# Kernel optimization log

Hardware: AMD Instinct MI355X
Metric: run time of the kernel (lower is better)

Reference implementation:

```python
import jax, jax.numpy as jnp
import numpy as np

B, S, HID = 4, 2048, 2048
H, KV, D = 16, 4, 128
G = H // KV  # kv groups
EPS = 1e-6
SCALE = D ** -0.5


def setup_inputs() -> dict:
    key = jax.random.key(0)
    ks = jax.random.split(key, 8)
    hidden_states = jax.random.normal(ks[0], (B, S, HID), jnp.float32)
    # real RoPE tables (rotate-half convention: freqs duplicated across halves)
    inv_freq = 1.0 / (10000.0 ** (np.arange(0, D, 2, dtype=np.float32) / D))
    t = np.arange(S, dtype=np.float32)
    freqs = np.outer(t, inv_freq)                      # [S, D/2]
    emb = np.concatenate([freqs, freqs], axis=-1)      # [S, D]
    cos = jnp.asarray(np.cos(emb), jnp.float32)
    sin = jnp.asarray(np.sin(emb), jnp.float32)
    std = HID ** -0.5
    Wq = jax.random.normal(ks[1], (HID, H * D), jnp.float32) * std
    Wk = jax.random.normal(ks[2], (HID, KV * D), jnp.float32) * std
    Wv = jax.random.normal(ks[3], (HID, KV * D), jnp.float32) * std
    Wo = jax.random.normal(ks[4], (H * D, HID), jnp.float32) * std
    q_norm_w = jnp.ones((D,), jnp.float32)
    k_norm_w = jnp.ones((D,), jnp.float32)
    return {"hidden_states": hidden_states, "cos": cos, "sin": sin,
            "Wq": Wq, "Wk": Wk, "Wv": Wv, "Wo": Wo,
            "q_norm_w": q_norm_w, "k_norm_w": k_norm_w}


def _rms_norm(x, w):
    xf = x.astype(jnp.float32)
    var = jnp.mean(xf * xf, axis=-1, keepdims=True)
    return w * (xf * jax.lax.rsqrt(var + EPS)).astype(x.dtype)


def _rotate_half(x):
    x1, x2 = x[..., : D // 2], x[..., D // 2:]
    return jnp.concatenate([-x2, x1], axis=-1)


def reference(hidden_states, cos, sin, Wq, Wk, Wv, Wo, q_norm_w, k_norm_w):
    x = hidden_states  # [B, S, HID]
    # projections + per-head RMSNorm
    q = _rms_norm((x @ Wq).reshape(B, S, H, D), q_norm_w).transpose(0, 2, 1, 3)   # [B,H,S,D]
    k = _rms_norm((x @ Wk).reshape(B, S, KV, D), k_norm_w).transpose(0, 2, 1, 3)  # [B,KV,S,D]
    v = (x @ Wv).reshape(B, S, KV, D).transpose(0, 2, 1, 3)                        # [B,KV,S,D]
    # RoPE (cos/sin broadcast [S,D] -> [B,heads,S,D])
    q = q * cos + _rotate_half(q) * sin
    k = k * cos + _rotate_half(k) * sin
    # GQA attention without materializing expanded K/V: group q heads per kv head
    qg = q.reshape(B, KV, G, S, D)
    scores = jnp.einsum('bkgsd,bktd->bkgst', qg, k) * SCALE       # [B,KV,G,S,S]
    probs = jax.nn.softmax(scores, axis=-1)
    out = jnp.einsum('bkgst,bktd->bkgsd', probs, v)               # [B,KV,G,S,D]
    out = out.reshape(B, H, S, D).transpose(0, 2, 1, 3).reshape(B, S, H * D)
    return out @ Wo
```

## Files before the change

kernel.cpp:

```cpp
#include <hip/hip_runtime.h>

#define DEVI __device__ __forceinline__

#define B_    4
#define S_    2048
#define HID_  2048
#define H_    16
#define KV_   4
#define D_    128
#define NQKV_ 3072
#define SCALE_ 0.08838834764831845f
#define L2E_   1.44269504088896340736f

typedef __bf16 bf16x8 __attribute__((ext_vector_type(8)));
typedef float  f32x4  __attribute__((ext_vector_type(4)));
typedef unsigned short ushort_t;

DEVI unsigned short f2bu(float f) {
  unsigned u = __float_as_uint(f);
  u += 0x7fffu + ((u >> 16) & 1u);
  return (unsigned short)(u >> 16);
}
DEVI float bu2f(unsigned short s) { return __uint_as_float(((unsigned)s) << 16); }
DEVI unsigned pk2(float a, float b) {
  return (unsigned)f2bu(a) | ((unsigned)f2bu(b) << 16);
}

DEVI void storev(ushort_t* p, float v) { *p = f2bu(v); }
DEVI void storev(float* p, float v)    { *p = v; }

DEVI void gl_lds16(const void* gptr, void* ldsptr) {
  __builtin_amdgcn_global_load_lds(
      (const __attribute__((address_space(1))) void*)gptr,
      (__attribute__((address_space(3))) void*)ldsptr, 16, 0, 0);
}

__global__ void k_cvt(const float* __restrict__ in, ushort_t* __restrict__ out, int n8) {
  int i = blockIdx.x * blockDim.x + threadIdx.x;
  if (i >= n8) return;
  const float4* p = (const float4*)in + (size_t)i * 2;
  float4 a = p[0], b = p[1];
  uint4 o;
  o.x = pk2(a.x, a.y);
  o.y = pk2(a.z, a.w);
  o.z = pk2(b.x, b.y);
  o.w = pk2(b.z, b.w);
  ((uint4*)out)[i] = o;
}

__global__ void k_transw(const float* __restrict__ in, ushort_t* __restrict__ out,
                         int K, int N) {
  __shared__ float tile[64][65];
  int k0 = blockIdx.x * 64, n0 = blockIdx.y * 64;
  int c = threadIdx.x & 63, r0 = threadIdx.x >> 6;
  #pragma unroll
  for (int i = 0; i < 16; ++i) {
    int r = r0 * 16 + i;
    tile[r][c] = in[(size_t)(k0 + r) * N + n0 + c];
  }
  __syncthreads();
  #pragma unroll
  for (int i = 0; i < 16; ++i) {
    int r = r0 * 16 + i;
    out[(size_t)(n0 + r) * K + k0 + c] = f2bu(tile[c][r]);
  }
}

__global__ void k_vtrans(const ushort_t* __restrict__ qkv, ushort_t* __restrict__ Vt) {
  __shared__ ushort_t tile[64][65];
  int s0 = blockIdx.x * 64, d0 = blockIdx.y * 64;
  int bkv = blockIdx.z, b = bkv >> 2, vh = bkv & 3;
  int c = threadIdx.x & 63, r0 = (threadIdx.x >> 6) * 16;
  const ushort_t* src = qkv + (size_t)(b * S_ + s0) * NQKV_ + 2560 + vh * 128 + d0;
  #pragma unroll
  for (int i = 0; i < 16; ++i) {
    int r = r0 + i;
    tile[r][c] = src[(size_t)r * NQKV_ + c];
  }
  __syncthreads();
  ushort_t* dst = Vt + ((size_t)(b * KV_ + vh) * D_ + d0) * S_ + s0;
  #pragma unroll
  for (int i = 0; i < 16; ++i) {
    int r = r0 + i;
    dst[(size_t)r * S_ + c] = tile[c][r];
  }
}

template <typename OutT>
__global__ __launch_bounds__(256)
void k_gemm(const ushort_t* __restrict__ A, const ushort_t* __restrict__ Bt,
            OutT* __restrict__ C, int M, int N, int K) {
  __shared__ __align__(16) ushort_t As[128 * 64];
  __shared__ __align__(16) ushort_t Bs[128 * 64];
  const int tid = threadIdx.x;
  const int wave = tid >> 6, lane = tid & 63;
  const int wr = wave >> 1, wc = wave & 1;
  const int h4 = lane >> 4, c16 = lane & 15;
  const int m0 = blockIdx.x * 128, n0 = blockIdx.y * 128;

  const int srow  = wave * 8 + (lane >> 3);
  const int scolb = (lane & 7) * 16;

  const ushort_t* Ap = A  + (size_t)m0 * K;
  const ushort_t* Bp = Bt + (size_t)n0 * K;

  f32x4 acc[4][4] = {};

  for (int kt = 0; kt < K; kt += 64) {
    __syncthreads();
    #pragma unroll
    for (int p = 0; p < 4; ++p) {
      int row = p * 32 + srow;
      gl_lds16((const char*)(Ap + (size_t)row * K + kt) + scolb,
               (char*)As + p * 4096 + wave * 1024);
      gl_lds16((const char*)(Bp + (size_t)row * K + kt) + scolb,
               (char*)Bs + p * 4096 + wave * 1024);
    }
    __syncthreads();
    #pragma unroll
    for (int kc = 0; kc < 2; ++kc) {
      bf16x8 af[4], bfr[4];
      #pragma unroll
      for (int m = 0; m < 4; ++m)
        af[m] = *(const bf16x8*)((const char*)As + (wr * 64 + m * 16 + c16) * 128 + kc * 64 + h4 * 16);
      #pragma unroll
      for (int n = 0; n < 4; ++n)
        bfr[n] = *(const bf16x8*)((const char*)Bs + (wc * 64 + n * 16 + c16) * 128 + kc * 64 + h4 * 16);
      #pragma unroll
      for (int m = 0; m < 4; ++m)
        #pragma unroll
        for (int n = 0; n < 4; ++n)
          acc[m][n] = __builtin_amdgcn_mfma_f32_16x16x32_bf16(af[m], bfr[n], acc[m][n], 0, 0, 0);
    }
  }
  #pragma unroll
  for (int m = 0; m < 4; ++m)
    #pragma unroll
    for (int n = 0; n < 4; ++n)
      #pragma unroll
      for (int r = 0; r < 4; ++r) {
        int grow = m0 + wr * 64 + m * 16 + h4 * 4 + r;
        int gcol = n0 + wc * 64 + n * 16 + c16;
        storev(&C[(size_t)grow * N + gcol], acc[m][n][r]);
      }
}

__global__ void k_normrope(const ushort_t* __restrict__ qkv,
                           const float* __restrict__ cosT, const float* __restrict__ sinT,
                           const float* __restrict__ qw, const float* __restrict__ kw,
                           ushort_t* __restrict__ Qr,
                           ushort_t* __restrict__ Kr) {
  int wid = blockIdx.x * 4 + (threadIdx.x >> 6);
  int lane = threadIdx.x & 63;
  int sub = wid % 20;
  int bs = wid / 20;
  int b = bs >> 11, s = bs & 2047;
  bool isQ = sub < 16;
  int head = isQ ? sub : sub - 16;
  const ushort_t* rp = qkv + (size_t)bs * NQKV_ + (isQ ? head * 128 : 2048 + head * 128);
  float e0 = bu2f(rp[lane]);
  float e1 = bu2f(rp[lane + 64]);
  float ss2 = e0 * e0 + e1 * e1;
  #pragma unroll
  for (int off = 32; off; off >>= 1) ss2 += __shfl_xor(ss2, off);
  float rinv = rsqrtf(ss2 * (1.0f / 128.0f) + 1e-6f);
  const float* w = isQ ? qw : kw;
  float y0 = e0 * rinv * w[lane];
  float y1 = e1 * rinv * w[lane + 64];
  float c0 = cosT[s * 128 + lane],      sn0 = sinT[s * 128 + lane];
  float c1 = cosT[s * 128 + lane + 64], sn1 = sinT[s * 128 + lane + 64];
  float o0 = y0 * c0 - y1 * sn0;
  float o1 = y1 * c1 + y0 * sn1;
  if (isQ) { o0 *= SCALE_; o1 *= SCALE_; }
  ushort_t* op = isQ ? (Qr + ((size_t)(b * H_ + head) * S_ + s) * D_)
                     : (Kr + ((size_t)(b * KV_ + head) * S_ + s) * D_);
  op[lane]      = f2bu(o0);
  op[lane + 64] = f2bu(o1);
}

__global__ __launch_bounds__(256)
void k_attn(const ushort_t* __restrict__ Qr, const ushort_t* __restrict__ Kr,
            const ushort_t* __restrict__ Vt, ushort_t* __restrict__ AO) {
  __shared__ __align__(16) ushort_t Ks[2][64 * 128];
  __shared__ __align__(16) ushort_t Vs[2][64 * 128];
  const int bh = blockIdx.y;
  const int b = bh >> 4, h = bh & 15, kvh = h >> 2;
  const int q0 = blockIdx.x * 64;
  const int tid = threadIdx.x;
  const int wave = tid >> 6, lane = tid & 63;
  const int h4 = lane >> 4, c16 = lane & 15;

  const ushort_t* qp = Qr + ((size_t)(b * H_ + h) * S_ + q0 + wave * 16 + c16) * D_;
  bf16x8 qf[4];
  #pragma unroll
  for (int kc = 0; kc < 4; ++kc)
    qf[kc] = *(const bf16x8*)(qp + kc * 32 + h4 * 8);

  const ushort_t* Kg = Kr + (size_t)(b * KV_ + kvh) * S_ * D_;
  const ushort_t* Vg = Vt + (size_t)(b * KV_ + kvh) * D_ * S_;

  const int soff = wave * 1024 + lane * 16;

  float mrow = -1e30f, lsum = 0.0f;
  f32x4 Of[8] = {};

#define STAGE(bufi, s0)                                                        \
  {                                                                            \
    _Pragma("unroll")                                                          \
    for (int p = 0; p < 4; ++p) {                                              \
      int off = p * 4096 + soff;                                               \
      int krow = off >> 8, kcolb = off & 255;                                  \
      int ksc = kcolb ^ ((krow & 7) << 4);                                     \
      gl_lds16((const char*)(Kg + (size_t)((s0) + krow) * D_) + ksc,           \
               (char*)Ks[bufi] + p * 4096 + wave * 1024);                      \
      int vrow = off >> 7, vcolb = off & 127;                                  \
      int vsc = vcolb ^ ((vrow & 7) << 4);                                     \
      gl_lds16((const char*)(Vg + (size_t)vrow * S_ + (s0)) + vsc,             \
               (char*)Vs[bufi] + p * 4096 + wave * 1024);                      \
    }                                                                          \
  }

  STAGE(0, 0);
  asm volatile("s_waitcnt vmcnt(0)" ::: "memory");
  __builtin_amdgcn_s_barrier();

  const int srcA = (2 * (h4 & 1)) * 16 + c16;
  const int srcB = srcA + 16;
  const bool hiKvt = (h4 >> 1) != 0;

  for (int nt = 0; nt < S_ / 64; ++nt) {
    const int cur = nt & 1;
    if (nt + 1 < S_ / 64) STAGE(cur ^ 1, (nt + 1) * 64);

    f32x4 st[4] = {};
    #pragma unroll
    for (int kvt = 0; kvt < 4; ++kvt) {
      const int krow = kvt * 16 + c16;
      const int xr = (krow & 7) << 4;
      #pragma unroll
      for (int kc = 0; kc < 4; ++kc) {
        bf16x8 kf = *(const bf16x8*)((const char*)Ks[cur] + krow * 256 +
                                     ((kc * 64 + h4 * 16) ^ xr));
        st[kvt] = __builtin_amdgcn_mfma_f32_16x16x32_bf16(kf, qf[kc], st[kvt], 0, 0, 0);
      }
    }

    float tmax = -1e30f;
    #pragma unroll
    for (int kvt = 0; kvt < 4; ++kvt)
      #pragma unroll
      for (int r = 0; r < 4; ++r) tmax = fmaxf(tmax, st[kvt][r]);
    tmax = fmaxf(tmax, __shfl_xor(tmax, 16));
    tmax = fmaxf(tmax, __shfl_xor(tmax, 32));
    const float mnew = fmaxf(mrow, tmax);
    const float corr = exp2f((mrow - mnew) * L2E_);
    mrow = mnew;

    float psum = 0.0f;
    unsigned pu[4][2];
    #pragma unroll
    for (int kvt = 0; kvt < 4; ++kvt) {
      float p0 = exp2f((st[kvt][0] - mnew) * L2E_);
      float p1 = exp2f((st[kvt][1] - mnew) * L2E_);
      float p2 = exp2f((st[kvt][2] - mnew) * L2E_);
      float p3 = exp2f((st[kvt][3] - mnew) * L2E_);
      psum += (p0 + p1) + (p2 + p3);
      pu[kvt][0] = pk2(p0, p1);
      pu[kvt][1] = pk2(p2, p3);
    }
    lsum = lsum * corr + psum;

    #pragma unroll
    for (int dt = 0; dt < 8; ++dt)
      #pragma unroll
      for (int r = 0; r < 4; ++r) Of[dt][r] *= corr;

    #pragma unroll
    for (int kvc = 0; kvc < 2; ++kvc) {
      unsigned w0a = __shfl(pu[kvc * 2][0], srcA), w0b = __shfl(pu[kvc * 2 + 1][0], srcA);
      unsigned w1a = __shfl(pu[kvc * 2][1], srcA), w1b = __shfl(pu[kvc * 2 + 1][1], srcA);
      unsigned w2a = __shfl(pu[kvc * 2][0], srcB), w2b = __shfl(pu[kvc * 2 + 1][0], srcB);
      unsigned w3a = __shfl(pu[kvc * 2][1], srcB), w3b = __shfl(pu[kvc * 2 + 1][1], srcB);
      uint4 pw;
      pw.x = hiKvt ? w0b : w0a;
      pw.y = hiKvt ? w1b : w1a;
      pw.z = hiKvt ? w2b : w2a;
      pw.w = hiKvt ? w3b : w3a;
      bf16x8 pb = __builtin_bit_cast(bf16x8, pw);
      #pragma unroll
      for (int dt = 0; dt < 8; ++dt) {
        const int vrow = dt * 16 + c16;
        bf16x8 vb = *(const bf16x8*)((const char*)Vs[cur] + vrow * 128 +
                                     ((kvc * 64 + h4 * 16) ^ ((vrow & 7) << 4)));
        Of[dt] = __builtin_amdgcn_mfma_f32_16x16x32_bf16(vb, pb, Of[dt], 0, 0, 0);
      }
    }

    asm volatile("s_waitcnt vmcnt(0)" ::: "memory");
    __builtin_amdgcn_s_barrier();
  }
#undef STAGE

  lsum += __shfl_xor(lsum, 16);
  lsum += __shfl_xor(lsum, 32);
  const float inv = 1.0f / lsum;

  const int s = q0 + wave * 16 + c16;
  ushort_t* aop = AO + ((size_t)(b * S_ + s) * H_ + h) * D_;
  #pragma unroll
  for (int dt = 0; dt < 8; ++dt) {
    const int d0 = dt * 16 + h4 * 4;
    *(unsigned*)(aop + d0)     = pk2(Of[dt][0] * inv, Of[dt][1] * inv);
    *(unsigned*)(aop + d0 + 2) = pk2(Of[dt][2] * inv, Of[dt][3] * inv);
  }
}

extern "C" void kernel_launch(void* const* d_in, const int* in_sizes, int n_in,
                              void* d_out, int out_size, void* d_ws, size_t ws_size,
                              hipStream_t stream) {
  const float* x    = (const float*)d_in[0];
  const float* cosT = (const float*)d_in[1];
  const float* sinT = (const float*)d_in[2];
  const float* Wq   = (const float*)d_in[3];
  const float* Wk   = (const float*)d_in[4];
  const float* Wv   = (const float*)d_in[5];
  const float* Wo   = (const float*)d_in[6];
  const float* qw   = (const float*)d_in[7];
  const float* kw   = (const float*)d_in[8];
  float* out = (float*)d_out;

  char* ws = (char*)d_ws;
  ushort_t* Xb    = (ushort_t*)(ws + 0);
  ushort_t* QKVt  = (ushort_t*)(ws + 33554432);
  ushort_t* Wtqkv = (ushort_t*)(ws + 83886080);
  ushort_t* Wto   = (ushort_t*)(ws + 96468992);
  ushort_t* Kr    = (ushort_t*)(ws + 104857600);
  ushort_t* Vt    = (ushort_t*)(ws + 113246208);
  ushort_t* Qr = Xb;
  ushort_t* AO = QKVt;

  k_cvt<<<8192, 256, 0, stream>>>(x, Xb, 2097152);
  k_transw<<<dim3(32, 32), 256, 0, stream>>>(Wq, Wtqkv, 2048, 2048);
  k_transw<<<dim3(32, 8),  256, 0, stream>>>(Wk, Wtqkv + (size_t)2048 * 2048, 2048, 512);
  k_transw<<<dim3(32, 8),  256, 0, stream>>>(Wv, Wtqkv + (size_t)2560 * 2048, 2048, 512);
  k_transw<<<dim3(32, 32), 256, 0, stream>>>(Wo, Wto, 2048, 2048);
  k_gemm<ushort_t><<<dim3(64, 24), 256, 0, stream>>>(Xb, Wtqkv, QKVt, 8192, 3072, 2048);
  k_normrope<<<40960, 256, 0, stream>>>(QKVt, cosT, sinT, qw, kw, Qr, Kr);
  k_vtrans<<<dim3(32, 2, 16), 256, 0, stream>>>(QKVt, Vt);
  k_attn<<<dim3(32, 64), 256, 0, stream>>>(Qr, Kr, Vt, AO);
  k_gemm<float><<<dim3(64, 16), 256, 0, stream>>>(AO, Wto, out, 8192, 2048, 2048);
}
```

Measured before the change: 741.5 us.

## Rework attention to 32x32 MFMA tiles with 128-query blocks and lazy rescaling

The attention kernel now uses 32x32x16 bf16 MFMA instead of 16x16x32, and each wave handles 32 query rows, so a block covers 128 queries and the grid is halved. This reuses each staged K/V tile across twice as many queries. The log2(e) factor is folded into the Q scaling during norm/RoPE, removing a multiply per exponent. The online-softmax rescale is skipped unless the row maximum rises by more than 8. P fragments are rearranged with v_permlane32_swap instead of shuffles, and setprio and launch bounds are added around the MFMA sections. The larger tiles raise register pressure, and the lazy rescale lets exponents reach up to 2^8, which could cost bf16 precision.

```diff
diff --git a/kernel.cpp b/kernel.cpp
--- a/kernel.cpp
+++ b/kernel.cpp
@@ -14,6 +14,7 @@
 
 typedef __bf16 bf16x8 __attribute__((ext_vector_type(8)));
 typedef float  f32x4  __attribute__((ext_vector_type(4)));
+typedef float  f32x16 __attribute__((ext_vector_type(16)));
 typedef unsigned short ushort_t;
 
 DEVI unsigned short f2bu(float f) {
@@ -171,30 +172,30 @@
   float c1 = cosT[s * 128 + lane + 64], sn1 = sinT[s * 128 + lane + 64];
   float o0 = y0 * c0 - y1 * sn0;
   float o1 = y1 * c1 + y0 * sn1;
-  if (isQ) { o0 *= SCALE_; o1 *= SCALE_; }
+  if (isQ) { o0 *= (SCALE_ * L2E_); o1 *= (SCALE_ * L2E_); }
   ushort_t* op = isQ ? (Qr + ((size_t)(b * H_ + head) * S_ + s) * D_)
                      : (Kr + ((size_t)(b * KV_ + head) * S_ + s) * D_);
   op[lane]      = f2bu(o0);
   op[lane + 64] = f2bu(o1);
 }
 
-__global__ __launch_bounds__(256)
+__global__ __launch_bounds__(256, 2)
 void k_attn(const ushort_t* __restrict__ Qr, const ushort_t* __restrict__ Kr,
             const ushort_t* __restrict__ Vt, ushort_t* __restrict__ AO) {
   __shared__ __align__(16) ushort_t Ks[2][64 * 128];
-  __shared__ __align__(16) ushort_t Vs[2][64 * 128];
+  __shared__ __align__(16) ushort_t Vs[2][128 * 64];
   const int bh = blockIdx.y;
   const int b = bh >> 4, h = bh & 15, kvh = h >> 2;
-  const int q0 = blockIdx.x * 64;
+  const int q0 = blockIdx.x * 128;
   const int tid = threadIdx.x;
   const int wave = tid >> 6, lane = tid & 63;
-  const int h4 = lane >> 4, c16 = lane & 15;
-
-  const ushort_t* qp = Qr + ((size_t)(b * H_ + h) * S_ + q0 + wave * 16 + c16) * D_;
-  bf16x8 qf[4];
-  #pragma unroll
-  for (int kc = 0; kc < 4; ++kc)
-    qf[kc] = *(const bf16x8*)(qp + kc * 32 + h4 * 8);
+  const int l31 = lane & 31, hi = lane >> 5;
+
+  const ushort_t* qp = Qr + ((size_t)(b * H_ + h) * S_ + q0 + wave * 32 + l31) * D_;
+  bf16x8 qf[8];
+  #pragma unroll
+  for (int kc = 0; kc < 8; ++kc)
+    qf[kc] = *(const bf16x8*)(qp + kc * 16 + hi * 8);
 
   const ushort_t* Kg = Kr + (size_t)(b * KV_ + kvh) * S_ * D_;
   const ushort_t* Vg = Vt + (size_t)(b * KV_ + kvh) * D_ * S_;
@@ -202,7 +203,7 @@
   const int soff = wave * 1024 + lane * 16;
 
   float mrow = -1e30f, lsum = 0.0f;
-  f32x4 Of[8] = {};
+  f32x16 Of[4] = {};
 
 #define STAGE(bufi, s0)                                                        \
   {                                                                            \
@@ -224,76 +225,75 @@
   asm volatile("s_waitcnt vmcnt(0)" ::: "memory");
   __builtin_amdgcn_s_barrier();
 
-  const int srcA = (2 * (h4 & 1)) * 16 + c16;
-  const int srcB = srcA + 16;
-  const bool hiKvt = (h4 >> 1) != 0;
-
   for (int nt = 0; nt < S_ / 64; ++nt) {
     const int cur = nt & 1;
     if (nt + 1 < S_ / 64) STAGE(cur ^ 1, (nt + 1) * 64);
 
-    f32x4 st[4] = {};
-    #pragma unroll
-    for (int kvt = 0; kvt < 4; ++kvt) {
-      const int krow = kvt * 16 + c16;
-      const int xr = (krow & 7) << 4;
-      #pragma unroll
-      for (int kc = 0; kc < 4; ++kc) {
-        bf16x8 kf = *(const bf16x8*)((const char*)Ks[cur] + krow * 256 +
-                                     ((kc * 64 + h4 * 16) ^ xr));
-        st[kvt] = __builtin_amdgcn_mfma_f32_16x16x32_bf16(kf, qf[kc], st[kvt], 0, 0, 0);
+    f32x16 st[2] = {};
+    __builtin_amdgcn_s_setprio(1);
+    #pragma unroll
+    for (int t = 0; t < 2; ++t) {
+      const int row = t * 32 + l31;
+      const int xr = (row & 7) << 4;
+      #pragma unroll
+      for (int kc = 0; kc < 8; ++kc) {
+        bf16x8 kf = *(const bf16x8*)((const char*)Ks[cur] + row * 256 +
+                                     ((kc * 32 + hi * 16) ^ xr));
+        st[t] = __builtin_amdgcn_mfma_f32_32x32x16_bf16(kf, qf[kc], st[t], 0, 0, 0);
       }
     }
-
-    float tmax = -1e30f;
-    #pragma unroll
-    for (int kvt = 0; kvt < 4; ++kvt)
-      #pragma unroll
-      for (int r = 0; r < 4; ++r) tmax = fmaxf(tmax, st[kvt][r]);
-    tmax = fmaxf(tmax, __shfl_xor(tmax, 16));
+    __builtin_amdgcn_s_setprio(0);
+
+    float tmax = st[0][0];
+    #pragma unroll
+    for (int r = 1; r < 16; ++r) tmax = fmaxf(tmax, st[0][r]);
+    #pragma unroll
+    for (int r = 0; r < 16; ++r) tmax = fmaxf(tmax, st[1][r]);
     tmax = fmaxf(tmax, __shfl_xor(tmax, 32));
-    const float mnew = fmaxf(mrow, tmax);
-    const float corr = exp2f((mrow - mnew) * L2E_);
-    mrow = mnew;
+
+    if (!__all(tmax - mrow <= 8.0f)) {
+      const float mnew = fmaxf(mrow, tmax);
+      const float corr = exp2f(mrow - mnew);
+      #pragma unroll
+      for (int dt = 0; dt < 4; ++dt)
+        #pragma unroll
+        for (int r = 0; r < 16; ++r) Of[dt][r] *= corr;
+      lsum *= corr;
+      mrow = mnew;
+    }
 
     float psum = 0.0f;
-    unsigned pu[4][2];
-    #pragma unroll
-    for (int kvt = 0; kvt < 4; ++kvt) {
-      float p0 = exp2f((st[kvt][0] - mnew) * L2E_);
-      float p1 = exp2f((st[kvt][1] - mnew) * L2E_);
-      float p2 = exp2f((st[kvt][2] - mnew) * L2E_);
-      float p3 = exp2f((st[kvt][3] - mnew) * L2E_);
-      psum += (p0 + p1) + (p2 + p3);
-      pu[kvt][0] = pk2(p0, p1);
-      pu[kvt][1] = pk2(p2, p3);
-    }
-    lsum = lsum * corr + psum;
-
-    #pragma unroll
-    for (int dt = 0; dt < 8; ++dt)
-      #pragma unroll
-      for (int r = 0; r < 4; ++r) Of[dt][r] *= corr;
-
-    #pragma unroll
-    for (int kvc = 0; kvc < 2; ++kvc) {
-      unsigned w0a = __shfl(pu[kvc * 2][0], srcA), w0b = __shfl(pu[kvc * 2 + 1][0], srcA);
-      unsigned w1a = __shfl(pu[kvc * 2][1], srcA), w1b = __shfl(pu[kvc * 2 + 1][1], srcA);
-      unsigned w2a = __shfl(pu[kvc * 2][0], srcB), w2b = __shfl(pu[kvc * 2 + 1][0], srcB);
-      unsigned w3a = __shfl(pu[kvc * 2][1], srcB), w3b = __shfl(pu[kvc * 2 + 1][1], srcB);
-      uint4 pw;
-      pw.x = hiKvt ? w0b : w0a;
-      pw.y = hiKvt ? w1b : w1a;
-      pw.z = hiKvt ? w2b : w2a;
-      pw.w = hiKvt ? w3b : w3a;
+    unsigned u[16];
+    #pragma unroll
+    for (int t = 0; t < 2; ++t)
+      #pragma unroll
+      for (int j = 0; j < 8; ++j) {
+        float pa = exp2f(st[t][2 * j]     - mrow);
+        float pb = exp2f(st[t][2 * j + 1] - mrow);
+        psum += pa + pb;
+        unsigned short xa = __builtin_bit_cast(unsigned short, (__bf16)pa);
+        unsigned short xb = __builtin_bit_cast(unsigned short, (__bf16)pb);
+        u[t * 8 + j] = (unsigned)xa | ((unsigned)xb << 16);
+      }
+    lsum += psum;
+
+    #pragma unroll
+    for (int kt = 0; kt < 4; ++kt) {
+      const int base = (kt >> 1) * 8 + (kt & 1) * 4;
+      unsigned w0 = u[base], w1 = u[base + 1], w2 = u[base + 2], w3 = u[base + 3];
+      asm("v_permlane32_swap_b32 %0, %1" : "+v"(w0), "+v"(w2));
+      asm("v_permlane32_swap_b32 %0, %1" : "+v"(w1), "+v"(w3));
+      uint4 pw; pw.x = w0; pw.y = w1; pw.z = w2; pw.w = w3;
       bf16x8 pb = __builtin_bit_cast(bf16x8, pw);
-      #pragma unroll
-      for (int dt = 0; dt < 8; ++dt) {
-        const int vrow = dt * 16 + c16;
-        bf16x8 vb = *(const bf16x8*)((const char*)Vs[cur] + vrow * 128 +
-                                     ((kvc * 64 + h4 * 16) ^ ((vrow & 7) << 4)));
-        Of[dt] = __builtin_amdgcn_mfma_f32_16x16x32_bf16(vb, pb, Of[dt], 0, 0, 0);
+      __builtin_amdgcn_s_setprio(1);
+      #pragma unroll
+      for (int dt = 0; dt < 4; ++dt) {
+        const int row = dt * 32 + l31;
+        bf16x8 vb = *(const bf16x8*)((const char*)Vs[cur] + row * 128 +
+                                     ((kt * 32 + hi * 16) ^ ((row & 7) << 4)));
+        Of[dt] = __builtin_amdgcn_mfma_f32_32x32x16_bf16(vb, pb, Of[dt], 0, 0, 0);
       }
+      __builtin_amdgcn_s_setprio(0);
     }
 
     asm volatile("s_waitcnt vmcnt(0)" ::: "memory");
@@ -301,18 +301,22 @@
   }
 #undef STAGE
 
-  lsum += __shfl_xor(lsum, 16);
   lsum += __shfl_xor(lsum, 32);
   const float inv = 1.0f / lsum;
 
-  const int s = q0 + wave * 16 + c16;
+  const int s = q0 + wave * 32 + l31;
   ushort_t* aop = AO + ((size_t)(b * S_ + s) * H_ + h) * D_;
   #pragma unroll
-  for (int dt = 0; dt < 8; ++dt) {
-    const int d0 = dt * 16 + h4 * 4;
-    *(unsigned*)(aop + d0)     = pk2(Of[dt][0] * inv, Of[dt][1] * inv);
-    *(unsigned*)(aop + d0 + 2) = pk2(Of[dt][2] * inv, Of[dt][3] * inv);
-  }
+  for (int dt = 0; dt < 4; ++dt)
+    #pragma unroll
+    for (int g = 0; g < 4; ++g) {
+      const int d0 = dt * 32 + g * 8 + hi * 4;
+      const int r0 = g * 4;
+      uint2 o;
+      o.x = pk2(Of[dt][r0]     * inv, Of[dt][r0 + 1] * inv);
+      o.y = pk2(Of[dt][r0 + 2] * inv, Of[dt][r0 + 3] * inv);
+      *(uint2*)(aop + d0) = o;
+    }
 }
 
 extern "C" void kernel_launch(void* const* d_in, const int* in_sizes, int n_in,
@@ -347,6 +351,6 @@
   k_gemm<ushort_t><<<dim3(64, 24), 256, 0, stream>>>(Xb, Wtqkv, QKVt, 8192, 3072, 2048);
   k_normrope<<<40960, 256, 0, stream>>>(QKVt, cosT, sinT, qw, kw, Qr, Kr);
   k_vtrans<<<dim3(32, 2, 16), 256, 0, stream>>>(QKVt, Vt);
-  k_attn<<<dim3(32, 64), 256, 0, stream>>>(Qr, Kr, Vt, AO);
+  k_attn<<<dim3(16, 64), 256, 0, stream>>>(Qr, Kr, Vt, AO);
   k_gemm<float><<<dim3(64, 16), 256, 0, stream>>>(AO, Wto, out, 8192, 2048, 2048);
 }
```

Result: faster. 619.9 us (-16.4%).
